# Performance work log

Measured on AMD Instinct MI355X. Metric: run time of the kernel, lower is better.

The kernel has to match this reference:

```python
import jax, jax.numpy as jnp
from jax import lax
import numpy as np

B, IMG_H, IMG_W = 8, 256, 512
NUM_CLASSES, P = 20, 32
SCALE, TOPK, IOU_THR = 32.0, 100, 0.5


def conv2d(x, w, b, stride=1, pad=1):
    y = lax.conv_general_dilated(x, w, (stride, stride), [(pad, pad), (pad, pad)],
                                 dimension_numbers=('NCHW', 'OIHW', 'NCHW'))
    return y + b[None, :, None, None]


def bilinear_resize(img, out_h, out_w):
    # img: [..., H, W]; torch F.interpolate(mode='bilinear', align_corners=False)
    H, W = img.shape[-2], img.shape[-1]
    def idx_w(n_in, n_out):
        src = (jnp.arange(n_out, dtype=jnp.float32) + 0.5) * (n_in / n_out) - 0.5
        src = jnp.clip(src, 0.0, n_in - 1)
        i0 = jnp.floor(src).astype(jnp.int32)
        i1 = jnp.minimum(i0 + 1, n_in - 1)
        return i0, i1, src - i0.astype(jnp.float32)
    y0, y1, wy = idx_w(H, out_h)
    x0, x1, wx = idx_w(W, out_w)
    top = img[..., y0, :] * (1.0 - wy)[:, None] + img[..., y1, :] * wy[:, None]
    return top[..., x0] * (1.0 - wx) + top[..., x1] * wx


def generate_anchors(fh, fw):
    ys = (jnp.arange(fh, dtype=jnp.float32) + 0.5) * (IMG_H / fh)
    xs = (jnp.arange(fw, dtype=jnp.float32) + 0.5) * (IMG_W / fw)
    cy, cx = jnp.meshgrid(ys, xs, indexing='ij')
    h = SCALE / 2
    return jnp.stack([cx - h, cy - h, cx + h, cy + h], -1).reshape(-1, 4)


def delta_to_boxes(anchors, deltas):
    a_c = (anchors[:, :2] + anchors[:, 2:]) / 2
    a_wh = anchors[:, 2:] - anchors[:, :2]
    pc = a_c + deltas[..., :2] * a_wh
    pwh = a_wh * jnp.exp(deltas[..., 2:])
    return jnp.concatenate([pc - pwh / 2, pc + pwh / 2], -1)


def nms_single(boxes, scores, labels):
    # torchvision batched_nms: offset boxes per label, greedy NMS, return kept idxs
    N = boxes.shape[0]
    off = labels.astype(boxes.dtype) * (jnp.max(boxes) + 1.0)
    b = boxes + off[:, None]
    order = jnp.argsort(-scores)
    bs = b[order]
    area = (bs[:, 2] - bs[:, 0]) * (bs[:, 3] - bs[:, 1])
    lt = jnp.maximum(bs[:, None, :2], bs[None, :, :2])
    rb = jnp.minimum(bs[:, None, 2:], bs[None, :, 2:])
    wh = jnp.clip(rb - lt, 0.0)
    inter = wh[..., 0] * wh[..., 1]
    iou = inter / (area[:, None] + area[None, :] - inter + 1e-9)
    idxs = jnp.arange(N)
    def body(i, suppressed):
        keep_i = jnp.logical_not(suppressed[i])
        row = (iou[i] > IOU_THR) & (idxs > i)
        return jnp.where(keep_i, suppressed | row, suppressed)
    suppressed = lax.fori_loop(0, N, body, jnp.zeros(N, bool))
    keep_mask = ~suppressed
    rank = jnp.cumsum(keep_mask) - 1
    slots = jnp.where(keep_mask & (rank < TOPK), rank, TOPK)
    out = jnp.full(TOPK + 1, -1, jnp.int32).at[slots].set(order.astype(jnp.int32))
    return out[:TOPK]


def setup_inputs():
    key = jax.random.key(0)
    ks = jax.random.split(key, 17)
    def cw(k, o, i, kh, kw_):
        return jax.random.normal(k, (o, i, kh, kw_), jnp.float32) / np.sqrt(i * kh * kw_)
    return {
        'images': jax.random.normal(ks[0], (B, 3, IMG_H, IMG_W), jnp.float32),
        'w1': cw(ks[1], 64, 3, 3, 3),   'b1': jnp.zeros(64, jnp.float32),
        'w2': cw(ks[2], 128, 64, 3, 3), 'b2': jnp.zeros(128, jnp.float32),
        'w3': cw(ks[3], 256, 128, 3, 3),'b3': jnp.zeros(256, jnp.float32),
        'pw1': cw(ks[4], 256, 256, 3, 3), 'pb1': jnp.zeros(256, jnp.float32),
        'pw2': cw(ks[5], P, 256, 1, 1),   'pb2': jnp.zeros(P, jnp.float32),
        'cw_': cw(ks[6], NUM_CLASSES + 1, 256, 3, 3), 'cb': jnp.zeros(NUM_CLASSES + 1, jnp.float32),
        'bw': cw(ks[7], 4, 256, 3, 3),  'bb': jnp.zeros(4, jnp.float32),
        'kw': cw(ks[8], P, 256, 3, 3),  'kb': jnp.zeros(P, jnp.float32),
    }


def reference(images, w1, b1, w2, b2, w3, b3, pw1, pb1, pw2, pb2, cw_, cb, bw, bb, kw, kb):
    x = jax.nn.relu(conv2d(images, w1, b1, stride=2))
    x = jax.nn.relu(conv2d(x, w2, b2, stride=2))
    feat = jax.nn.relu(conv2d(x, w3, b3, stride=2))          # [B,256,32,64]
    proto = conv2d(jax.nn.relu(conv2d(feat, pw1, pb1)), pw2, pb2, pad=0)  # [B,P,32,64]
    fh, fw = feat.shape[2], feat.shape[3]
    def head(w, b, c):
        return conv2d(feat, w, b).transpose(0, 2, 3, 1).reshape(B, -1, c)
    cls = head(cw_, cb, NUM_CLASSES + 1)     # [B,N,C+1]
    box = head(bw, bb, 4)                    # [B,N,4]
    coef = head(kw, kb, P)                   # [B,N,P]
    anchors = generate_anchors(fh, fw)       # [N,4]
    probs = jax.nn.softmax(cls, -1)[..., :-1]
    scores = probs.max(-1)
    labels = probs.argmax(-1).astype(jnp.int32)
    boxes = delta_to_boxes(anchors, box)     # [B,N,4]
    keep = jax.vmap(nms_single)(boxes, scores, labels)   # [B,100], -1 pad
    valid = keep >= 0
    ki = jnp.clip(keep, 0)
    take = lambda a: jnp.take_along_axis(a, ki[..., None] if a.ndim == 3 else ki, axis=1)
    boxes_k = take(boxes) * valid[..., None]
    scores_k = take(scores) * valid
    labels_k = jnp.where(valid, take(labels), 0)
    coef_k = jnp.take_along_axis(coef, ki[..., None], axis=1)   # [B,100,P]
    m = jax.nn.sigmoid(jnp.einsum('bkp,bphw->bkhw', coef_k, proto))
    masks = bilinear_resize(m, IMG_H, IMG_W) > 0.5
    masks = masks & valid[..., None, None]
    return boxes_k, scores_k, labels_k, masks, valid
```

## Files before the change

kernel.cpp:

```cpp
#include <hip/hip_runtime.h>
#include <hip/hip_bf16.h>
#include <math.h>

#define BB 8
#define NCLS 21
#define NANCH 2048
#define TOPK_N 100

static const size_t OFF_X1HI = 0;
static const size_t OFF_X1LO = 34344960;
static const size_t OFF_X2HI = 68689920;
static const size_t OFF_X2LO = 86261760;
static const size_t OFF_FTHI = 103833600;
static const size_t OFF_FTLO = 113025024;
static const size_t OFF_WT1  = 122216448;
static const size_t OFF_A2H  = 122223616;
static const size_t OFF_A2L  = 122371072;
static const size_t OFF_A3H  = 122518528;
static const size_t OFF_A3L  = 123108352;
static const size_t OFF_AHH  = 123698176;
static const size_t OFF_AHL  = 123993088;
static const size_t OFF_AP1H = 124288000;
static const size_t OFF_AP1L = 125467648;
static const size_t OFF_WTP2 = 126647296;
static const size_t OFF_BH   = 126680064;
static const size_t OFF_HOUT = 126680576;
static const size_t OFF_P1   = 130874880;
static const size_t OFF_PROTO= 147652096;
static const size_t OFF_BOXES= 149749248;
static const size_t OFF_SCORES=150011392;
static const size_t OFF_LABELS=150076928;
static const size_t OFF_ORDER= 150142464;
static const size_t OFF_SB   = 150208000;
static const size_t OFF_IOU  = 150470144;
static const size_t OFF_KEEP = 154664448;
static const size_t OFF_MAXB = 154668032;

static const size_t OUT_BOXES  = 0;
static const size_t OUT_SCORES = 3200;
static const size_t OUT_LABELS = 4000;
static const size_t OUT_MASKS  = 4800;
static const size_t OUT_VALID  = 104862400;

typedef __attribute__((ext_vector_type(8))) short bf16x8;
typedef __attribute__((ext_vector_type(4))) float f32x4;

__device__ __forceinline__ unsigned encf(float f){
  unsigned u = __float_as_uint(f);
  return (u & 0x80000000u) ? ~u : (u | 0x80000000u);
}
__device__ __forceinline__ float decf(unsigned u){
  unsigned b = (u & 0x80000000u) ? (u & 0x7fffffffu) : ~u;
  return __uint_as_float(b);
}
__device__ __forceinline__ short f2bf(float f){
  __hip_bfloat16 h = __float2bfloat16(f);
  return *(short*)&h;
}
__device__ __forceinline__ float bf2f(short h){
  return __uint_as_float(((unsigned)(unsigned short)h) << 16);
}

__global__ void halok3(short* __restrict__ x1hi, short* __restrict__ x1lo,
                       short* __restrict__ x2hi, short* __restrict__ x2lo,
                       short* __restrict__ fthi, short* __restrict__ ftlo,
                       unsigned* __restrict__ maxb){
  int i = blockIdx.x*256 + threadIdx.x;
  if (i < BB) maxb[i] = 0u;
  short *hi, *lo; int Hp, Wp, cell, bg;
  if (i < 49408){
    hi=x1hi; lo=x1lo; Hp=130; Wp=258; cell = i % 772; bg = i / 772;
  } else if (i < 99072){
    int j = i - 49408; hi=x2hi; lo=x2lo; Hp=66; Wp=130; cell = j % 388; bg = j / 388;
  } else if (i < 149248){
    int j = i - 99072; hi=fthi; lo=ftlo; Hp=34; Wp=66; cell = j % 196; bg = j / 196;
  } else return;
  int y, x;
  if (cell < Wp)        { y = 0;      x = cell; }
  else if (cell < 2*Wp) { y = Hp-1;   x = cell - Wp; }
  else { int r = cell - 2*Wp; y = 1 + (r>>1); x = (r&1) ? (Wp-1) : 0; }
  size_t ad = (((size_t)bg*Hp + y)*Wp + x)*8;
  bf16x8 z = (bf16x8){0,0,0,0,0,0,0,0};
  *(bf16x8*)(hi + ad) = z;
  *(bf16x8*)(lo + ad) = z;
}

template<int CIN,int COUT,int KK>
__device__ __forceinline__ void packw_body(int i, const float* __restrict__ w,
                                           float* __restrict__ wT){
  if (i >= CIN*KK*COUT) return;
  int co = i % COUT; int r = i / COUT;
  int ci = r / KK,  k = r % KK;
  wT[i] = w[(co*CIN + ci)*KK + k];
}

template<int CIN,int COUT>
__device__ __forceinline__ void packA_body(int i, const float* __restrict__ w,
                                           short* __restrict__ Ahi, short* __restrict__ Alo){
  constexpr int K = CIN*9;
  constexpr int KS = K/32;
  if (i >= COUT*K) return;
  int sub  = i & 7;
  int lane = (i >> 3) & 63;
  int rest = i >> 9;
  int ks = rest % KS;
  int mt = rest / KS;
  int m = mt*16 + (lane & 15);
  int k = ks*32 + (lane >> 4)*8 + sub;
  int tap = k / CIN, ci = k - tap*CIN;
  float v = w[(m*CIN + ci)*9 + tap];
  short h = f2bf(v);
  Ahi[i] = h;
  Alo[i] = f2bf(v - bf2f(h));
}

__device__ __forceinline__ void packAh_body(int i,
    const float* __restrict__ cw, const float* __restrict__ bw,
    const float* __restrict__ kw, const float* __restrict__ cb,
    const float* __restrict__ bb, const float* __restrict__ kb,
    short* __restrict__ Ahi, short* __restrict__ Alo, float* __restrict__ bh){
  if (i < 64){
    float v = 0.f;
    if (i < 21) v = cb[i]; else if (i < 25) v = bb[i-21]; else if (i < 57) v = kb[i-25];
    bh[i] = v;
  }
  if (i >= 64*2304) return;
  constexpr int KS = 72;
  int sub  = i & 7;
  int lane = (i >> 3) & 63;
  int rest = i >> 9;
  int ks = rest % KS;
  int mt = rest / KS;
  int m = mt*16 + (lane & 15);
  int k = ks*32 + (lane >> 4)*8 + sub;
  int tap = k >> 8, ci = k & 255;
  float v = 0.f;
  if (m < 21)      v = cw[(m*256 + ci)*9 + tap];
  else if (m < 25) v = bw[((m-21)*256 + ci)*9 + tap];
  else if (m < 57) v = kw[((m-25)*256 + ci)*9 + tap];
  short h = f2bf(v);
  Ahi[i] = h;
  Alo[i] = f2bf(v - bf2f(h));
}

__global__ void packall(const float* __restrict__ w1, float* __restrict__ wT1,
                        const float* __restrict__ w2, short* __restrict__ a2h, short* __restrict__ a2l,
                        const float* __restrict__ w3, short* __restrict__ a3h, short* __restrict__ a3l,
                        const float* __restrict__ pw1, short* __restrict__ ap1h, short* __restrict__ ap1l,
                        const float* __restrict__ cw, const float* __restrict__ bw,
                        const float* __restrict__ kw, const float* __restrict__ cb,
                        const float* __restrict__ bb, const float* __restrict__ kb,
                        short* __restrict__ ahh, short* __restrict__ ahl, float* __restrict__ bh,
                        const float* __restrict__ pw2, float* __restrict__ wTp2){
  int blk = blockIdx.x, t = threadIdx.x;
  if (blk < 288)        packA_body<64,128>(blk*256+t, w2, a2h, a2l);
  else if (blk < 1440)  packA_body<128,256>((blk-288)*256+t, w3, a3h, a3l);
  else if (blk < 3744)  packA_body<256,256>((blk-1440)*256+t, pw1, ap1h, ap1l);
  else if (blk < 4320)  packAh_body((blk-3744)*256+t, cw,bw,kw,cb,bb,kb, ahh,ahl,bh);
  else if (blk < 4327)  packw_body<3,64,9>((blk-4320)*256+t, w1, wT1);
  else                  packw_body<256,32,1>((blk-4327)*256+t, pw2, wTp2);
}

__global__ __launch_bounds__(256) void conv1k(const float* __restrict__ img,
    const float* __restrict__ wT, const float* __restrict__ bias,
    short* __restrict__ x1hi, short* __restrict__ x1lo){
  const int b   = blockIdx.z;
  const int co0 = blockIdx.y * 16;
  const int g   = blockIdx.x*256 + threadIdx.x;
  const int y  = g >> 7;
  const int x0 = (g & 127) << 1;

  float acc[16][2];
#pragma unroll
  for (int c=0;c<16;c++){
    float bv = bias[co0+c];
    acc[c][0] = bv; acc[c][1] = bv;
  }
  int   off[3][5];
  float msk[3][5];
#pragma unroll
  for (int kh=0;kh<3;kh++){
    int iy = y*2 - 1 + kh;
    bool okr = (iy >= 0) && (iy < 256);
    int ro = okr ? iy*512 : 0;
#pragma unroll
    for (int t=0;t<5;t++){
      int col = x0*2 - 1 + t;
      bool ok = okr && (col >= 0) && (col < 512);
      off[kh][t] = ok ? (ro + col) : 0;
      msk[kh][t] = ok ? 1.f : 0.f;
    }
  }
  const float* inb = img + (size_t)b*3*256*512;
  for (int ci=0; ci<3; ci++){
    const float* inc = inb + (size_t)ci*256*512;
    float v[3][5];
#pragma unroll
    for (int kh=0;kh<3;kh++)
#pragma unroll
      for (int t=0;t<5;t++)
        v[kh][t] = inc[off[kh][t]] * msk[kh][t];
    const float* wp = wT + ci*9*64 + co0;
#pragma unroll
    for (int kh=0;kh<3;kh++)
#pragma unroll
    for (int kw=0;kw<3;kw++){
      const float* wq = wp + (kh*3+kw)*64;
#pragma unroll
      for (int c=0;c<16;c++){
        float wv = wq[c];
        acc[c][0] = fmaf(wv, v[kh][2*0+kw], acc[c][0]);
        acc[c][1] = fmaf(wv, v[kh][2*1+kw], acc[c][1]);
      }
    }
  }
#pragma unroll
  for (int s=0;s<2;s++){
    short hv[16] __attribute__((aligned(16)));
    short lv[16] __attribute__((aligned(16)));
#pragma unroll
    for (int c=0;c<16;c++){
      float r = fmaxf(acc[c][s], 0.f);
      short h = f2bf(r);
      hv[c] = h;
      lv[c] = f2bf(r - bf2f(h));
    }
#pragma unroll
    for (int g2=0; g2<2; g2++){
      size_t ad = (((size_t)(b*8 + (co0>>3) + g2)*130 + (y+1))*258 + (x0+s+1))*8;
      *(bf16x8*)(x1hi + ad) = *(bf16x8*)(hv + g2*8);
      *(bf16x8*)(x1lo + ad) = *(bf16x8*)(lv + g2*8);
    }
  }
}

template<int CIN,int K,int M,int MW,int NW,int S,int IPH,int IPW,int NXB,
         bool SPLIT,bool STAGELO,int EMODE,int OPH,int OPW>
__global__ __launch_bounds__(NW*64) void cgemm_row(
    const short* __restrict__ Ahi, const short* __restrict__ Alo,
    const short* __restrict__ Bhi, const short* __restrict__ Blo,
    const float* __restrict__ bias, float* __restrict__ outf,
    short* __restrict__ outhi, short* __restrict__ outlo){
  static_assert(CIN % 32 == 0, "CIN must be multiple of 32");
  constexpr int NT = 64*32;
  constexpr int KS = K/32;
  constexpr int CG = CIN/8;
  constexpr int SW  = 64*S + 2;
  constexpr int SWP = (S==2) ? (SW/2 + 1) : SW;
  constexpr int PARS = (S==2) ? 2 : 1;
  constexpr int LOOFF = CG*PARS*SWP*8;
  constexpr int BUFS = (SPLIT && STAGELO) ? 2 : 1;
  __shared__ __align__(16) short sB[BUFS*LOOFF];

  const int b    = blockIdx.z;
  const int oy   = blockIdx.x / NXB;
  const int xb   = (blockIdx.x % NXB) * 64;
  const int wave = threadIdx.x >> 6;
  const int lane = threadIdx.x & 63;
  const int lm = lane & 15, lq = lane >> 4;
  const int m0 = (blockIdx.y * NW + wave) * (MW*16);
  const int tid = threadIdx.x;

  f32x4 acc[MW][4];
#pragma unroll
  for (int i=0;i<MW;i++)
#pragma unroll
    for (int j=0;j<4;j++) acc[i][j] = (f32x4){0.f,0.f,0.f,0.f};

  const short* Ah_l = Ahi + (size_t)lane*8;
  const short* Al_l = Alo + (size_t)lane*8;
  const int mt0 = m0 >> 4;
  const size_t plane = (size_t)IPH*IPW;
  const short* Bl0 = Blo + ((size_t)b*CG + lq)*plane*8;

#pragma unroll 1
  for (int dy=0; dy<3; dy++){
    const int iy = oy*S + dy;
    __syncthreads();
    {
      const short* srch = Bhi + (((size_t)b*CG*IPH + iy)*IPW + (size_t)(xb*S))*8;
      for (int c = tid; c < CG*SW; c += NW*64){
        int g = c / SW, p = c - g*SW;
        int dst = (S==2) ? ((g*2 + (p&1))*SWP + (p>>1)) : (g*SW + p);
        *(bf16x8*)(&sB[(size_t)dst*8]) =
          *(const bf16x8*)(srch + ((size_t)g*plane + p)*8);
      }
      if constexpr (SPLIT && STAGELO){
        const short* srcl = Blo + (((size_t)b*CG*IPH + iy)*IPW + (size_t)(xb*S))*8;
        for (int c = tid; c < CG*SW; c += NW*64){
          int g = c / SW, p = c - g*SW;
          int dst = (S==2) ? ((g*2 + (p&1))*SWP + (p>>1)) : (g*SW + p);
          *(bf16x8*)(&sB[LOOFF + (size_t)dst*8]) =
            *(const bf16x8*)(srcl + ((size_t)g*plane + p)*8);
        }
      }
    }
    __syncthreads();
#pragma unroll
    for (int dx=0; dx<3; dx++){
      const int tap = dy*3 + dx;
      const int ksb = tap*(CIN/32);
      for (int kc=0; kc<CIN; kc+=32){
        const int ks = ksb + (kc>>5);
        int ra[4];
#pragma unroll
        for (int j=0;j<4;j++){
          int pc = (j*16 + lm)*S + dx;
          ra[j] = (S==2) ? ((((kc>>3) + lq)*2 + (pc&1))*SWP + (pc>>1))
                         : (((kc>>3) + lq)*SW + pc);
        }
        bf16x8 ah[MW], bh_[4];
#pragma unroll
        for (int i=0;i<MW;i++)
          ah[i] = *(const bf16x8*)(Ah_l + ((size_t)(mt0+i)*KS + ks)*512);
#pragma unroll
        for (int j=0;j<4;j++)
          bh_[j] = *(const bf16x8*)(&sB[(size_t)ra[j]*8]);
        if constexpr (SPLIT){
          bf16x8 al[MW], bl_[4];
#pragma unroll
          for (int i=0;i<MW;i++)
            al[i] = *(const bf16x8*)(Al_l + ((size_t)(mt0+i)*KS + ks)*512);
          if constexpr (STAGELO){
#pragma unroll
            for (int j=0;j<4;j++)
              bl_[j] = *(const bf16x8*)(&sB[LOOFF + (size_t)ra[j]*8]);
          } else {
#pragma unroll
            for (int j=0;j<4;j++){
              size_t pix = (size_t)iy*IPW + (size_t)((xb + j*16 + lm)*S + dx);
              bl_[j] = *(const bf16x8*)(Bl0 + ((size_t)(kc>>3)*plane + pix)*8);
            }
          }
#pragma unroll
          for (int j=0;j<4;j++)
#pragma unroll
            for (int i=0;i<MW;i++)
              acc[i][j] = __builtin_amdgcn_mfma_f32_16x16x32_bf16(ah[i], bh_[j], acc[i][j], 0,0,0);
#pragma unroll
          for (int j=0;j<4;j++)
#pragma unroll
            for (int i=0;i<MW;i++)
              acc[i][j] = __builtin_amdgcn_mfma_f32_16x16x32_bf16(ah[i], bl_[j], acc[i][j], 0,0,0);
#pragma unroll
          for (int j=0;j<4;j++)
#pragma unroll
            for (int i=0;i<MW;i++)
              acc[i][j] = __builtin_amdgcn_mfma_f32_16x16x32_bf16(al[i], bh_[j], acc[i][j], 0,0,0);
        } else {
#pragma unroll
          for (int j=0;j<4;j++)
#pragma unroll
            for (int i=0;i<MW;i++)
              acc[i][j] = __builtin_amdgcn_mfma_f32_16x16x32_bf16(ah[i], bh_[j], acc[i][j], 0,0,0);
        }
      }
    }
  }

#pragma unroll
  for (int i=0;i<MW;i++){
#pragma unroll
    for (int r=0;r<4;r++){
      const int m = m0 + i*16 + lq*4 + r;
      const float bv = bias[m];
      if constexpr (EMODE == 0){
#pragma unroll
        for (int j=0;j<4;j++){
          const int ox = xb + j*16 + lm;
          float v = fmaxf(acc[i][j][r] + bv, 0.f);
          short h = f2bf(v);
          short l = f2bf(v - bf2f(h));
          size_t ad = ((((size_t)(b*(M/8) + (m>>3))*OPH + (oy+1))*OPW + (ox+1)))*8 + (m&7);
          outhi[ad] = h;
          outlo[ad] = l;
        }
      } else {
        float* cp = outf + ((size_t)b*M + m)*NT + oy*64 + lm;
#pragma unroll
        for (int j=0;j<4;j++){
          float v = acc[i][j][r] + bv;
          if constexpr (EMODE == 2) v = fmaxf(v, 0.f);
          cp[j*16] = v;
        }
      }
    }
  }
}

__global__ __launch_bounds__(256) void headspw1(
    const short* __restrict__ Ahh, const short* __restrict__ Ahl,
    const short* __restrict__ Aph,
    const short* __restrict__ Bhi, const short* __restrict__ Blo,
    const float* __restrict__ biash, const float* __restrict__ biasp,
    float* __restrict__ hout, float* __restrict__ p1){
  constexpr int KS = 72;
  constexpr int CG = 32;
  constexpr int SW = 66;
  constexpr int IPH = 34, IPW = 66;
  constexpr int LOOFF = CG*SW*8;
  __shared__ __align__(16) short sB[2*LOOFF];

  const int b = blockIdx.z;
  const int oy = blockIdx.x;
  const int wave = threadIdx.x >> 6;
  const int lane = threadIdx.x & 63;
  const int lm = lane & 15, lq = lane >> 4;
  const int tid = threadIdx.x;

  f32x4 acch[4];
  f32x4 accp[4][4];
#pragma unroll
  for (int j=0;j<4;j++) acch[j] = (f32x4){0.f,0.f,0.f,0.f};
#pragma unroll
  for (int i=0;i<4;i++)
#pragma unroll
    for (int j=0;j<4;j++) accp[i][j] = (f32x4){0.f,0.f,0.f,0.f};

  const short* Ah_l = Ahh + (size_t)lane*8;
  const short* Al_l = Ahl + (size_t)lane*8;
  const short* Ap_l = Aph + (size_t)lane*8;
  const size_t plane = (size_t)IPH*IPW;

#pragma unroll 1
  for (int dy=0; dy<3; dy++){
    const int iy = oy + dy;
    __syncthreads();
    {
      const short* srch = Bhi + ((size_t)b*CG*IPH + iy)*IPW*8;
      const short* srcl = Blo + ((size_t)b*CG*IPH + iy)*IPW*8;
      for (int c = tid; c < CG*SW; c += 256){
        int g = c / SW, p = c - g*SW;
        *(bf16x8*)(&sB[(size_t)c*8]) =
          *(const bf16x8*)(srch + ((size_t)g*plane + p)*8);
        *(bf16x8*)(&sB[LOOFF + (size_t)c*8]) =
          *(const bf16x8*)(srcl + ((size_t)g*plane + p)*8);
      }
    }
    __syncthreads();
#pragma unroll
    for (int dx=0; dx<3; dx++){
      const int tap = dy*3 + dx;
      const int ksb = tap*8;
      for (int kc=0; kc<256; kc+=32){
        const int ks = ksb + (kc>>5);
        int ra[4];
#pragma unroll
        for (int j=0;j<4;j++) ra[j] = ((kc>>3) + lq)*SW + (j*16 + lm) + dx;
        bf16x8 bh_[4], bl_[4];
#pragma unroll
        for (int j=0;j<4;j++){
          bh_[j] = *(const bf16x8*)(&sB[(size_t)ra[j]*8]);
          bl_[j] = *(const bf16x8*)(&sB[LOOFF + (size_t)ra[j]*8]);
        }
        bf16x8 ah = *(const bf16x8*)(Ah_l + ((size_t)wave*KS + ks)*512);
        bf16x8 al = *(const bf16x8*)(Al_l + ((size_t)wave*KS + ks)*512);
#pragma unroll
        for (int j=0;j<4;j++)
          acch[j] = __builtin_amdgcn_mfma_f32_16x16x32_bf16(ah, bh_[j], acch[j], 0,0,0);
#pragma unroll
        for (int j=0;j<4;j++)
          acch[j] = __builtin_amdgcn_mfma_f32_16x16x32_bf16(ah, bl_[j], acch[j], 0,0,0);
#pragma unroll
        for (int j=0;j<4;j++)
          acch[j] = __builtin_amdgcn_mfma_f32_16x16x32_bf16(al, bh_[j], acch[j], 0,0,0);
#pragma unroll
        for (int i=0;i<4;i++){
          bf16x8 ap = *(const bf16x8*)(Ap_l + ((size_t)(wave*4+i)*KS + ks)*512);
#pragma unroll
          for (int j=0;j<4;j++)
            accp[i][j] = __builtin_amdgcn_mfma_f32_16x16x32_bf16(ap, bh_[j], accp[i][j], 0,0,0);
        }
      }
    }
  }

#pragma unroll
  for (int r=0;r<4;r++){
    const int mh = wave*16 + lq*4 + r;
    const float bv = biash[mh];
    float* cp = hout + ((size_t)b*64 + mh)*NANCH + oy*64 + lm;
#pragma unroll
    for (int j=0;j<4;j++) cp[j*16] = acch[j][r] + bv;
  }
#pragma unroll
  for (int i=0;i<4;i++){
#pragma unroll
    for (int r=0;r<4;r++){
      const int mp = wave*64 + i*16 + lq*4 + r;
      const float bv = biasp[mp];
      float* cp = p1 + ((size_t)b*256 + mp)*NANCH + oy*64 + lm;
#pragma unroll
      for (int j=0;j<4;j++) cp[j*16] = fmaxf(accp[i][j][r] + bv, 0.f);
    }
  }
}

__global__ __launch_bounds__(256) void pw2k2(const float* __restrict__ p1,
    const float* __restrict__ wT, const float* __restrict__ bias,
    float* __restrict__ proto){
  const int b  = blockIdx.y;
  const int sp = blockIdx.x*256 + threadIdx.x;
  float acc[32];
#pragma unroll
  for (int c=0;c<32;c++) acc[c] = bias[c];
  const float* pb = p1 + (size_t)b*256*NANCH + sp;
  for (int ci=0;ci<256;ci++){
    float v = pb[(size_t)ci*NANCH];
    const float* wq = wT + ci*32;
#pragma unroll
    for (int c=0;c<32;c++) acc[c] = fmaf(v, wq[c], acc[c]);
  }
#pragma unroll
  for (int c=0;c<32;c++)
    proto[((size_t)b*32 + c)*NANCH + sp] = acc[c];
}

__global__ void decodek(const float* __restrict__ hout,
                        float* __restrict__ boxes, float* __restrict__ scores,
                        int* __restrict__ labels, unsigned* __restrict__ maxb){
  const int b = blockIdx.y;
  const int n = blockIdx.x*blockDim.x + threadIdx.x;
  const float* cp = hout + (size_t)b*64*NANCH + n;
  float l[NCLS];
  float M = -1e30f;
#pragma unroll
  for (int c=0;c<NCLS;c++){ l[c] = cp[(size_t)c*NANCH]; M = fmaxf(M, l[c]); }
  float denom = 0.f;
#pragma unroll
  for (int c=0;c<NCLS;c++) denom += expf(l[c]-M);
  float best = -1.f; int bi = 0;
#pragma unroll
  for (int c=0;c<NCLS-1;c++){
    float e = expf(l[c]-M);
    if (e > best){ best = e; bi = c; }
  }
  scores[(size_t)b*NANCH + n] = best/denom;
  labels[(size_t)b*NANCH + n] = bi;

  float dx = cp[21*(size_t)NANCH], dy = cp[22*(size_t)NANCH];
  float dw = cp[23*(size_t)NANCH], dh = cp[24*(size_t)NANCH];
  const int yy = n >> 6, xx = n & 63;
  float cx = (xx+0.5f)*8.f, cy = (yy+0.5f)*8.f;
  float px = cx + dx*32.f, py = cy + dy*32.f;
  float pw = 32.f*expf(dw), ph = 32.f*expf(dh);
  float x1 = px - 0.5f*pw, y1 = py - 0.5f*ph;
  float x2 = px + 0.5f*pw, y2 = py + 0.5f*ph;
  float* bo = boxes + ((size_t)b*NANCH + n)*4;
  bo[0]=x1; bo[1]=y1; bo[2]=x2; bo[3]=y2;
  float mx = fmaxf(fmaxf(x1,y1), fmaxf(x2,y2));
#pragma unroll
  for (int off=32; off>0; off>>=1) mx = fmaxf(mx, __shfl_down(mx, off));
  if ((threadIdx.x & 63) == 0) atomicMax(maxb + b, encf(mx));
}

__global__ void __launch_bounds__(1024) sortk(const float* __restrict__ scores,
                     const float* __restrict__ boxes, const int* __restrict__ labels,
                     const unsigned* __restrict__ maxb,
                     int* __restrict__ order, float* __restrict__ sb){
  __shared__ float sc[NANCH];
  __shared__ int   id[NANCH];
  const int b = blockIdx.x, t = threadIdx.x;
  for (int i=t;i<NANCH;i+=1024){ sc[i]=scores[(size_t)b*NANCH+i]; id[i]=i; }
  __syncthreads();
  for (int k=2;k<=NANCH;k<<=1){
    for (int j=k>>1;j>0;j>>=1){
      for (int i=t;i<NANCH;i+=1024){
        int ixj = i ^ j;
        if (ixj > i){
          float sa=sc[i], sb_=sc[ixj]; int ia=id[i], ib=id[ixj];
          bool dir = ((i & k) == 0);
          bool before_ba = (sb_ > sa) || (sb_ == sa && ib < ia);
          if (before_ba == dir){ sc[i]=sb_; sc[ixj]=sa; id[i]=ib; id[ixj]=ia; }
        }
      }
      __syncthreads();
    }
  }
  float mboff = decf(maxb[b]) + 1.0f;
  for (int r=t;r<NANCH;r+=1024){
    int o = id[r];
    order[(size_t)b*NANCH + r] = o;
    float off = (float)labels[(size_t)b*NANCH + o] * mboff;
    const float* bo = boxes + ((size_t)b*NANCH + o)*4;
    float* sp = sb + ((size_t)b*NANCH + r)*4;
    sp[0]=bo[0]+off; sp[1]=bo[1]+off; sp[2]=bo[2]+off; sp[3]=bo[3]+off;
  }
}

__global__ void ioumask(const float* __restrict__ sb, unsigned long long* __restrict__ iou){
  const int b = blockIdx.y;
  const int gid = blockIdx.x*blockDim.x + threadIdx.x;
  const int i = gid >> 5, w = gid & 31;
  const float* base = sb + (size_t)b*NANCH*4;
  unsigned long long bits = 0ull;
  const int j0 = w << 6;
  if (j0 + 63 > i){
    float x1=base[i*4], y1=base[i*4+1], x2=base[i*4+2], y2=base[i*4+3];
    float ai = (x2-x1)*(y2-y1);
    for (int jj=0;jj<64;jj++){
      int j = j0 + jj;
      if (j > i){
        float bx1=base[j*4], by1=base[j*4+1], bx2=base[j*4+2], by2=base[j*4+3];
        float lx=fmaxf(x1,bx1), ly=fmaxf(y1,by1);
        float rx=fminf(x2,bx2), ry=fminf(y2,by2);
        float ww=fmaxf(rx-lx,0.f), hh=fmaxf(ry-ly,0.f);
        float inter = ww*hh;
        float aj = (bx2-bx1)*(by2-by1);
        float v = inter/(ai + aj - inter + 1e-9f);
        if (v > 0.5f) bits |= (1ull << jj);
      }
    }
  }
  iou[((size_t)b*NANCH + i)*32 + w] = bits;
}

__global__ void nmsgather(const unsigned long long* __restrict__ iou,
                          const int* __restrict__ order,
                          const float* __restrict__ boxes, const float* __restrict__ scores,
                          const int* __restrict__ labels,
                          int* __restrict__ keep, float* __restrict__ out){
  const int b = blockIdx.x, lane = threadIdx.x;
  __shared__ int s_keep[TOPK_N];
  unsigned long long sup = 0ull;
  int k = 0, i = 0;
  while (k < TOPK_N){
    unsigned long long avail = (lane < 32) ? ~sup : 0ull;
    const int wi = i >> 6;
    if (lane < wi) avail = 0ull;
    else if (lane == wi) avail &= (~0ull) << (i & 63);
    unsigned long long ball = __ballot(avail != 0ull);
    if (!ball) break;
    int w0 = (int)__builtin_ctzll(ball);
    unsigned long long aw = __shfl(avail, w0);
    int b0 = (int)__builtin_ctzll(aw);
    i = (w0 << 6) + b0;
    int ov = order[(size_t)b*NANCH + i];
    if (lane == 0) s_keep[k] = ov;
    k++;
    unsigned long long row = (lane < 32) ? iou[((size_t)b*NANCH + i)*32 + lane] : 0ull;
    sup |= row;
    i++;
    if (i >= NANCH) break;
  }
  __syncthreads();
  for (int r = lane; r < TOPK_N; r += 64){
    int kv = (r < k) ? s_keep[r] : -1;
    keep[b*TOPK_N + r] = kv;
    float valid = (kv >= 0) ? 1.f : 0.f;
    int kc = (kv < 0) ? 0 : kv;
    const float* bo = boxes + ((size_t)b*NANCH + kc)*4;
#pragma unroll
    for (int c=0;c<4;c++) out[OUT_BOXES + ((size_t)b*TOPK_N + r)*4 + c] = bo[c]*valid;
    out[OUT_SCORES + b*TOPK_N + r] = scores[(size_t)b*NANCH + kc]*valid;
    out[OUT_LABELS + b*TOPK_N + r] = (kv >= 0) ? (float)labels[(size_t)b*NANCH + kc] : 0.f;
    out[OUT_VALID  + b*TOPK_N + r] = valid;
  }
}

__global__ __launch_bounds__(256) void maskresize(const int* __restrict__ keep,
    const float* __restrict__ hout, const float* __restrict__ proto,
    float* __restrict__ out){
  const int b = blockIdx.y, r = blockIdx.x;
  float* obase = out + OUT_MASKS + ((size_t)b*TOPK_N + r)*131072;
  int ki = keep[b*TOPK_N + r];
  if (ki < 0){
    float4 z = make_float4(0.f,0.f,0.f,0.f);
    for (int idx = threadIdx.x; idx < 32768; idx += 256)
      ((float4*)obase)[idx] = z;
    return;
  }
  __shared__ float cf[32];
  __shared__ float sm[NANCH];
  if (threadIdx.x < 32)
    cf[threadIdx.x] = hout[((size_t)b*64 + 25 + threadIdx.x)*NANCH + ki];
  __syncthreads();
  for (int s = threadIdx.x; s < NANCH; s += 256){
    float acc = 0.f;
#pragma unroll
    for (int p=0;p<32;p++) acc = fmaf(cf[p], proto[((size_t)b*32 + p)*NANCH + s], acc);
    sm[s] = 1.f/(1.f + expf(-acc));
  }
  __syncthreads();
  for (int pid = threadIdx.x; pid < 32768; pid += 256){
    const int y  = pid >> 7;
    const int x4 = (pid & 127) << 2;
    float sy = (y + 0.5f)*0.125f - 0.5f;
    sy = fminf(fmaxf(sy, 0.f), 31.f);
    int y0 = (int)floorf(sy);
    int y1 = min(y0+1, 31);
    float wy = sy - (float)y0;
    const float* r0 = sm + y0*64;
    const float* r1 = sm + y1*64;
    float res[4];
#pragma unroll
    for (int kk=0;kk<4;kk++){
      int x = x4 + kk;
      float sx = (x + 0.5f)*0.125f - 0.5f;
      sx = fminf(fmaxf(sx, 0.f), 63.f);
      int x0 = (int)floorf(sx);
      int x1 = min(x0+1, 63);
      float wx = sx - (float)x0;
      float t0 = r0[x0]*(1.f-wy) + r1[x0]*wy;
      float t1 = r0[x1]*(1.f-wy) + r1[x1]*wy;
      float v  = t0*(1.f-wx) + t1*wx;
      res[kk] = (v > 0.5f) ? 1.f : 0.f;
    }
    *(float4*)(obase + y*512 + x4) = make_float4(res[0], res[1], res[2], res[3]);
  }
}

extern "C" void kernel_launch(void* const* d_in, const int* in_sizes, int n_in,
                              void* d_out, int out_size, void* d_ws, size_t ws_size,
                              hipStream_t stream) {
  const float* images=(const float*)d_in[0];
  const float* w1=(const float*)d_in[1];  const float* b1=(const float*)d_in[2];
  const float* w2=(const float*)d_in[3];  const float* b2=(const float*)d_in[4];
  const float* w3=(const float*)d_in[5];  const float* b3=(const float*)d_in[6];
  const float* pw1=(const float*)d_in[7]; const float* pb1=(const float*)d_in[8];
  const float* pw2=(const float*)d_in[9]; const float* pb2=(const float*)d_in[10];
  const float* cw=(const float*)d_in[11]; const float* cb=(const float*)d_in[12];
  const float* bw=(const float*)d_in[13]; const float* bb=(const float*)d_in[14];
  const float* kw=(const float*)d_in[15]; const float* kb=(const float*)d_in[16];
  float* out = (float*)d_out;
  char* ws = (char*)d_ws;

  short* x1hi = (short*)(ws + OFF_X1HI);
  short* x1lo = (short*)(ws + OFF_X1LO);
  short* x2hi = (short*)(ws + OFF_X2HI);
  short* x2lo = (short*)(ws + OFF_X2LO);
  short* fthi = (short*)(ws + OFF_FTHI);
  short* ftlo = (short*)(ws + OFF_FTLO);
  float* wT1  = (float*)(ws + OFF_WT1);
  short* a2h  = (short*)(ws + OFF_A2H);
  short* a2l  = (short*)(ws + OFF_A2L);
  short* a3h  = (short*)(ws + OFF_A3H);
  short* a3l  = (short*)(ws + OFF_A3L);
  short* ahh  = (short*)(ws + OFF_AHH);
  short* ahl  = (short*)(ws + OFF_AHL);
  short* ap1h = (short*)(ws + OFF_AP1H);
  short* ap1l = (short*)(ws + OFF_AP1L);
  float* wTp2 = (float*)(ws + OFF_WTP2);
  float* bh   = (float*)(ws + OFF_BH);
  float* hout = (float*)(ws + OFF_HOUT);
  float* p1   = (float*)(ws + OFF_P1);
  float* proto= (float*)(ws + OFF_PROTO);
  float* boxes= (float*)(ws + OFF_BOXES);
  float* scores=(float*)(ws + OFF_SCORES);
  int*   labels=(int*)  (ws + OFF_LABELS);
  int*   order =(int*)  (ws + OFF_ORDER);
  float* sb   = (float*)(ws + OFF_SB);
  unsigned long long* iou = (unsigned long long*)(ws + OFF_IOU);
  int*   keep = (int*)  (ws + OFF_KEEP);
  unsigned* maxb = (unsigned*)(ws + OFF_MAXB);

  halok3<<<dim3(583), 256, 0, stream>>>(x1hi, x1lo, x2hi, x2lo, fthi, ftlo, maxb);

  packall<<<dim3(4359), 256, 0, stream>>>(w1, wT1, w2, a2h, a2l, w3, a3h, a3l,
                                          pw1, ap1h, ap1l, cw, bw, kw, cb, bb, kb,
                                          ahh, ahl, bh, pw2, wTp2);

  conv1k<<<dim3(64,4,BB), 256, 0, stream>>>(images, wT1, b1, x1hi, x1lo);

  cgemm_row<64,576,128,2,4,2,130,258,2,true,true,0,66,130>
      <<<dim3(128,1,BB), 256, 0, stream>>>(a2h, a2l, x1hi, x1lo, b2, nullptr, x2hi, x2lo);

  cgemm_row<128,1152,256,2,8,2,66,130,1,true,true,0,34,66>
      <<<dim3(32,1,BB), 512, 0, stream>>>(a3h, a3l, x2hi, x2lo, b3, nullptr, fthi, ftlo);

  headspw1<<<dim3(32,1,BB), 256, 0, stream>>>(ahh, ahl, ap1h, fthi, ftlo,
                                              bh, pb1, hout, p1);

  pw2k2<<<dim3(8,BB), 256, 0, stream>>>(p1, wTp2, pb2, proto);

  decodek<<<dim3(8,BB), 256, 0, stream>>>(hout, boxes, scores, labels, maxb);
  sortk<<<dim3(BB), 1024, 0, stream>>>(scores, boxes, labels, maxb, order, sb);
  ioumask<<<dim3(256,BB), 256, 0, stream>>>(sb, iou);
  nmsgather<<<dim3(BB), 64, 0, stream>>>(iou, order, boxes, scores, labels, keep, out);

  maskresize<<<dim3(TOPK_N,BB), 256, 0, stream>>>(keep, hout, proto, out);
}
```

Measured before the change: 979.4 us.

## Split head/proto convs, fuse decode into head kernel, re-split conv3 grid

```diff
diff --git a/kernel.cpp b/kernel.cpp
--- a/kernel.cpp
+++ b/kernel.cpp
@@ -388,12 +388,12 @@
   }
 }
 
-__global__ __launch_bounds__(256) void headspw1(
-    const short* __restrict__ Ahh, const short* __restrict__ Ahl,
-    const short* __restrict__ Aph,
+__global__ __launch_bounds__(256) void headsdec(
+    const short* __restrict__ Ahi, const short* __restrict__ Alo,
     const short* __restrict__ Bhi, const short* __restrict__ Blo,
-    const float* __restrict__ biash, const float* __restrict__ biasp,
-    float* __restrict__ hout, float* __restrict__ p1){
+    const float* __restrict__ bias, float* __restrict__ hout,
+    float* __restrict__ boxes, float* __restrict__ scores,
+    int* __restrict__ labels, unsigned* __restrict__ maxb){
   constexpr int KS = 72;
   constexpr int CG = 32;
   constexpr int SW = 66;
@@ -401,25 +401,19 @@
   constexpr int LOOFF = CG*SW*8;
   __shared__ __align__(16) short sB[2*LOOFF];
 
-  const int b = blockIdx.z;
+  const int b  = blockIdx.z;
   const int oy = blockIdx.x;
   const int wave = threadIdx.x >> 6;
   const int lane = threadIdx.x & 63;
   const int lm = lane & 15, lq = lane >> 4;
   const int tid = threadIdx.x;
 
-  f32x4 acch[4];
-  f32x4 accp[4][4];
-#pragma unroll
-  for (int j=0;j<4;j++) acch[j] = (f32x4){0.f,0.f,0.f,0.f};
-#pragma unroll
-  for (int i=0;i<4;i++)
-#pragma unroll
-    for (int j=0;j<4;j++) accp[i][j] = (f32x4){0.f,0.f,0.f,0.f};
-
-  const short* Ah_l = Ahh + (size_t)lane*8;
-  const short* Al_l = Ahl + (size_t)lane*8;
-  const short* Ap_l = Aph + (size_t)lane*8;
+  f32x4 acc[4];
+#pragma unroll
+  for (int j=0;j<4;j++) acc[j] = (f32x4){0.f,0.f,0.f,0.f};
+
+  const short* Ah_l = Ahi + (size_t)lane*8;
+  const short* Al_l = Alo + (size_t)lane*8;
   const size_t plane = (size_t)IPH*IPW;
 
 #pragma unroll 1
@@ -457,42 +451,65 @@
         bf16x8 al = *(const bf16x8*)(Al_l + ((size_t)wave*KS + ks)*512);
 #pragma unroll
         for (int j=0;j<4;j++)
-          acch[j] = __builtin_amdgcn_mfma_f32_16x16x32_bf16(ah, bh_[j], acch[j], 0,0,0);
+          acc[j] = __builtin_amdgcn_mfma_f32_16x16x32_bf16(ah, bh_[j], acc[j], 0,0,0);
 #pragma unroll
         for (int j=0;j<4;j++)
-          acch[j] = __builtin_amdgcn_mfma_f32_16x16x32_bf16(ah, bl_[j], acch[j], 0,0,0);
+          acc[j] = __builtin_amdgcn_mfma_f32_16x16x32_bf16(ah, bl_[j], acc[j], 0,0,0);
 #pragma unroll
         for (int j=0;j<4;j++)
-          acch[j] = __builtin_amdgcn_mfma_f32_16x16x32_bf16(al, bh_[j], acch[j], 0,0,0);
-#pragma unroll
-        for (int i=0;i<4;i++){
-          bf16x8 ap = *(const bf16x8*)(Ap_l + ((size_t)(wave*4+i)*KS + ks)*512);
-#pragma unroll
-          for (int j=0;j<4;j++)
-            accp[i][j] = __builtin_amdgcn_mfma_f32_16x16x32_bf16(ap, bh_[j], accp[i][j], 0,0,0);
-        }
-      }
-    }
-  }
-
+          acc[j] = __builtin_amdgcn_mfma_f32_16x16x32_bf16(al, bh_[j], acc[j], 0,0,0);
+      }
+    }
+  }
+
+  __syncthreads();
+  float* sF = (float*)sB;
 #pragma unroll
   for (int r=0;r<4;r++){
-    const int mh = wave*16 + lq*4 + r;
-    const float bv = biash[mh];
-    float* cp = hout + ((size_t)b*64 + mh)*NANCH + oy*64 + lm;
-#pragma unroll
-    for (int j=0;j<4;j++) cp[j*16] = acch[j][r] + bv;
-  }
-#pragma unroll
-  for (int i=0;i<4;i++){
-#pragma unroll
-    for (int r=0;r<4;r++){
-      const int mp = wave*64 + i*16 + lq*4 + r;
-      const float bv = biasp[mp];
-      float* cp = p1 + ((size_t)b*256 + mp)*NANCH + oy*64 + lm;
-#pragma unroll
-      for (int j=0;j<4;j++) cp[j*16] = fmaxf(accp[i][j][r] + bv, 0.f);
-    }
+    const int m = wave*16 + lq*4 + r;
+    const float bv = bias[m];
+    float* cp = hout + ((size_t)b*64 + m)*NANCH + oy*64 + lm;
+#pragma unroll
+    for (int j=0;j<4;j++){
+      float v = acc[j][r] + bv;
+      cp[j*16] = v;
+      sF[m*68 + j*16 + lm] = v;
+    }
+  }
+  __syncthreads();
+
+  if (tid < 64){
+    const int n = oy*64 + tid;
+    float l[NCLS];
+    float M = -1e30f;
+#pragma unroll
+    for (int c=0;c<NCLS;c++){ l[c] = sF[c*68 + tid]; M = fmaxf(M, l[c]); }
+    float denom = 0.f;
+#pragma unroll
+    for (int c=0;c<NCLS;c++) denom += expf(l[c]-M);
+    float best = -1.f; int bi = 0;
+#pragma unroll
+    for (int c=0;c<NCLS-1;c++){
+      float e = expf(l[c]-M);
+      if (e > best){ best = e; bi = c; }
+    }
+    scores[(size_t)b*NANCH + n] = best/denom;
+    labels[(size_t)b*NANCH + n] = bi;
+
+    float dxv = sF[21*68 + tid], dyv = sF[22*68 + tid];
+    float dwv = sF[23*68 + tid], dhv = sF[24*68 + tid];
+    const int yy = n >> 6, xx = n & 63;
+    float cx = (xx+0.5f)*8.f, cy = (yy+0.5f)*8.f;
+    float px = cx + dxv*32.f, py = cy + dyv*32.f;
+    float pw = 32.f*expf(dwv), ph = 32.f*expf(dhv);
+    float x1 = px - 0.5f*pw, y1 = py - 0.5f*ph;
+    float x2 = px + 0.5f*pw, y2 = py + 0.5f*ph;
+    float* bo = boxes + ((size_t)b*NANCH + n)*4;
+    bo[0]=x1; bo[1]=y1; bo[2]=x2; bo[3]=y2;
+    float mx = fmaxf(fmaxf(x1,y1), fmaxf(x2,y2));
+#pragma unroll
+    for (int off=32; off>0; off>>=1) mx = fmaxf(mx, __shfl_down(mx, off));
+    if (tid == 0) atomicMax(maxb + b, encf(mx));
   }
 }
 
@@ -514,44 +531,6 @@
 #pragma unroll
   for (int c=0;c<32;c++)
     proto[((size_t)b*32 + c)*NANCH + sp] = acc[c];
-}
-
-__global__ void decodek(const float* __restrict__ hout,
-                        float* __restrict__ boxes, float* __restrict__ scores,
-                        int* __restrict__ labels, unsigned* __restrict__ maxb){
-  const int b = blockIdx.y;
-  const int n = blockIdx.x*blockDim.x + threadIdx.x;
-  const float* cp = hout + (size_t)b*64*NANCH + n;
-  float l[NCLS];
-  float M = -1e30f;
-#pragma unroll
-  for (int c=0;c<NCLS;c++){ l[c] = cp[(size_t)c*NANCH]; M = fmaxf(M, l[c]); }
-  float denom = 0.f;
-#pragma unroll
-  for (int c=0;c<NCLS;c++) denom += expf(l[c]-M);
-  float best = -1.f; int bi = 0;
-#pragma unroll
-  for (int c=0;c<NCLS-1;c++){
-    float e = expf(l[c]-M);
-    if (e > best){ best = e; bi = c; }
-  }
-  scores[(size_t)b*NANCH + n] = best/denom;
-  labels[(size_t)b*NANCH + n] = bi;
-
-  float dx = cp[21*(size_t)NANCH], dy = cp[22*(size_t)NANCH];
-  float dw = cp[23*(size_t)NANCH], dh = cp[24*(size_t)NANCH];
-  const int yy = n >> 6, xx = n & 63;
-  float cx = (xx+0.5f)*8.f, cy = (yy+0.5f)*8.f;
-  float px = cx + dx*32.f, py = cy + dy*32.f;
-  float pw = 32.f*expf(dw), ph = 32.f*expf(dh);
-  float x1 = px - 0.5f*pw, y1 = py - 0.5f*ph;
-  float x2 = px + 0.5f*pw, y2 = py + 0.5f*ph;
-  float* bo = boxes + ((size_t)b*NANCH + n)*4;
-  bo[0]=x1; bo[1]=y1; bo[2]=x2; bo[3]=y2;
-  float mx = fmaxf(fmaxf(x1,y1), fmaxf(x2,y2));
-#pragma unroll
-  for (int off=32; off>0; off>>=1) mx = fmaxf(mx, __shfl_down(mx, off));
-  if ((threadIdx.x & 63) == 0) atomicMax(maxb + b, encf(mx));
 }
 
 __global__ void __launch_bounds__(1024) sortk(const float* __restrict__ scores,
@@ -765,15 +744,17 @@
   cgemm_row<64,576,128,2,4,2,130,258,2,true,true,0,66,130>
       <<<dim3(128,1,BB), 256, 0, stream>>>(a2h, a2l, x1hi, x1lo, b2, nullptr, x2hi, x2lo);
 
-  cgemm_row<128,1152,256,2,8,2,66,130,1,true,true,0,34,66>
-      <<<dim3(32,1,BB), 512, 0, stream>>>(a3h, a3l, x2hi, x2lo, b3, nullptr, fthi, ftlo);
-
-  headspw1<<<dim3(32,1,BB), 256, 0, stream>>>(ahh, ahl, ap1h, fthi, ftlo,
-                                              bh, pb1, hout, p1);
+  cgemm_row<128,1152,256,2,4,2,66,130,1,true,true,0,34,66>
+      <<<dim3(32,2,BB), 256, 0, stream>>>(a3h, a3l, x2hi, x2lo, b3, nullptr, fthi, ftlo);
+
+  headsdec<<<dim3(32,1,BB), 256, 0, stream>>>(ahh, ahl, fthi, ftlo, bh, hout,
+                                              boxes, scores, labels, maxb);
+
+  cgemm_row<256,2304,256,2,4,1,34,66,1,false,false,2,1,1>
+      <<<dim3(32,2,BB), 256, 0, stream>>>(ap1h, ap1l, fthi, fthi, pb1, p1, nullptr, nullptr);
 
   pw2k2<<<dim3(8,BB), 256, 0, stream>>>(p1, wTp2, pb2, proto);
 
-  decodek<<<dim3(8,BB), 256, 0, stream>>>(hout, boxes, scores, labels, maxb);
   sortk<<<dim3(BB), 1024, 0, stream>>>(scores, boxes, labels, maxb, order, sb);
   ioumask<<<dim3(256,BB), 256, 0, stream>>>(sb, iou);
   nmsgather<<<dim3(BB), 64, 0, stream>>>(iou, order, boxes, scores, labels, keep, out);
```

Result: no change. 970.4 us (-0.9%).
